# Optimization experiments

Measured on AMD Instinct MI355X. Metric: run time of the kernel, lower is better.

Reference implementation:

```python
import jax, jax.numpy as jnp
import numpy as np

EPS = 1e-5
N_HEAD = 16

def _ln(x, g, b):
    m = jnp.mean(x, -1, keepdims=True)
    v = jnp.mean((x - m) ** 2, -1, keepdims=True)
    return (x - m) * jax.lax.rsqrt(v + EPS) * g + b

def _mlp(x, fc_w, fc_b, proj_w, proj_b):
    h = x @ fc_w.T + fc_b
    h = h * jax.nn.sigmoid(1.702 * h)  # QuickGELU
    return h @ proj_w.T + proj_b

def setup_inputs() -> dict:
    key = jax.random.key(0)
    ks = jax.random.split(key, 16)
    S, B, D, BOX = 577, 8, 1024, 16
    sc = 0.02
    return {
        'x': jax.random.normal(ks[0], (S, B, D), jnp.float32),
        'detection_attn_mask': jax.random.normal(ks[1], (B * BOX * N_HEAD, 1, S), jnp.float32),
        'box_coords': jax.random.uniform(ks[2], (B, BOX, 4), jnp.float32),
        'layers': 24,
        'need_patch': 0,
        'in_proj_w': sc * jax.random.normal(ks[3], (3 * D, D), jnp.float32),
        'in_proj_b': jnp.zeros((3 * D,), jnp.float32),
        'out_w': sc * jax.random.normal(ks[4], (D, D), jnp.float32),
        'out_b': jnp.zeros((D,), jnp.float32),
        'ln1_g': jnp.ones((D,), jnp.float32),
        'ln1_b': jnp.zeros((D,), jnp.float32),
        'ln2_g': jnp.ones((D,), jnp.float32),
        'ln2_b': jnp.zeros((D,), jnp.float32),
        'fc_w': sc * jax.random.normal(ks[5], (4 * D, D), jnp.float32),
        'fc_b': jnp.zeros((4 * D,), jnp.float32),
        'proj_w': sc * jax.random.normal(ks[6], (D, 4 * D), jnp.float32),
        'proj_b': jnp.zeros((D,), jnp.float32),
    }

def reference(x, detection_attn_mask, box_coords, layers, need_patch,
              in_proj_w, in_proj_b, out_w, out_b,
              ln1_g, ln1_b, ln2_g, ln2_b, fc_w, fc_b, proj_w, proj_b):
    # step == layers-1, detection_attn_mask is not None, need_patch is False.
    S, B, D = x.shape
    H = N_HEAD
    hd = D // H
    BOX = box_coords.shape[1]  # uniform boxes per image

    h = _ln(x, ln1_g, ln1_b)                       # [S,B,D]
    qkv = h @ in_proj_w.T + in_proj_b              # [S,B,3D]
    q, k, v = jnp.split(qkv, 3, axis=-1)

    # query is sliced to the CLS token only (q[:, :1, :] after head split)
    q0 = q[0].reshape(B, H, hd) / jnp.sqrt(jnp.asarray(hd, x.dtype))  # [B,H,hd]
    kh = k.reshape(S, B, H, hd).transpose(1, 2, 0, 3)                 # [B,H,S,hd]
    vh = v.reshape(S, B, H, hd).transpose(1, 2, 0, 3)                 # [B,H,S,hd]

    attn = jnp.einsum('bhe,bhse->bhs', q0, kh)     # [B,H,S]

    # mask rows are ordered (batch, box, head); Nt == 1 is squeezed
    mask = detection_attn_mask.reshape(B, BOX, H, S)
    p_exp = jax.nn.softmax(attn[:, None] + mask, axis=-1)             # [B,BOX,H,S]
    out_exp = jnp.einsum('bxhs,bhse->bxhe', p_exp, vh).reshape(B * BOX, D)
    out_exp = out_exp @ out_w.T + out_b            # [B*BOX, D]

    p = jax.nn.softmax(attn, axis=-1)
    out = jnp.einsum('bhs,bhse->bhe', p, vh).reshape(B, D) @ out_w.T + out_b

    cls = x[0] + out                               # residual with CLS token
    cls = cls + _mlp(_ln(cls, ln2_g, ln2_b), fc_w, fc_b, proj_w, proj_b)

    x0_exp = jnp.repeat(x[0], BOX, axis=0)         # [B*BOX, D], batch-major
    mask_cls = x0_exp + out_exp
    mask_cls = mask_cls + _mlp(_ln(mask_cls, ln2_g, ln2_b), fc_w, fc_b, proj_w, proj_b)

    return mask_cls[None], cls[None]               # [1,B*BOX,D], [1,B,D]
```

## Files before the change

kernel.cpp:

```cpp
#include <hip/hip_runtime.h>
#include <stdint.h>

typedef unsigned short u16;
typedef unsigned int u32;
typedef __bf16 bf16x8 __attribute__((ext_vector_type(8)));
typedef float f32x4 __attribute__((ext_vector_type(4)));

#define LDT 72
#define HLD 516

__device__ __forceinline__ float bf2f(u16 u) {
  u32 v = ((u32)u) << 16;
  return __builtin_bit_cast(float, v);
}
__device__ __forceinline__ u16 f2bf(float f) {
  u32 u = __builtin_bit_cast(u32, f);
  u32 r = u + 0x7fffu + ((u >> 16) & 1u);
  return (u16)(r >> 16);
}

__device__ __forceinline__ float block_sum4(float v, float* red, int t) {
#pragma unroll
  for (int o = 32; o; o >>= 1) v += __shfl_xor(v, o, 64);
  if ((t & 63) == 0) red[t >> 6] = v;
  __syncthreads();
  float r = red[0] + red[1] + red[2] + red[3];
  __syncthreads();
  return r;
}

#define GLD16(gp, lp)                                                   \
  __builtin_amdgcn_global_load_lds(                                     \
      (const __attribute__((address_space(1))) void*)(gp),              \
      (__attribute__((address_space(3))) void*)(lp), 16, 0, 0)

__global__ __launch_bounds__(256) void cvt_ln(
    const float* __restrict__ WV, u16* __restrict__ WVD,
    const float* __restrict__ X, const float* __restrict__ G,
    const float* __restrict__ Bt, u16* __restrict__ O) {
  int t = threadIdx.x;
  if (blockIdx.x < 1024) {
    int i = blockIdx.x * 1024 + t * 4;
    float4 f = *(const float4*)(WV + i);
    u32 lo = (u32)f2bf(f.x) | ((u32)f2bf(f.y) << 16);
    u32 hi = (u32)f2bf(f.z) | ((u32)f2bf(f.w) << 16);
    uint2 val = {lo, hi};
    *(uint2*)(WVD + i) = val;
    return;
  }
  __shared__ float red[4];
  int row = blockIdx.x - 1024;
  float4 xv = *(const float4*)(X + (size_t)row * 1024 + t * 4);
  float v[4] = {xv.x, xv.y, xv.z, xv.w};
  float s = v[0] + v[1] + v[2] + v[3];
  s = block_sum4(s, red, t);
  float mean = s * (1.f / 1024.f);
  float q = 0.f;
#pragma unroll
  for (int i = 0; i < 4; ++i) { float d = v[i] - mean; q += d * d; }
  q = block_sum4(q, red, t);
  float rstd = rsqrtf(q * (1.f / 1024.f) + 1e-5f);
  float4 g = *(const float4*)(G + t * 4);
  float4 b = *(const float4*)(Bt + t * 4);
  float gg[4] = {g.x, g.y, g.z, g.w}, bb[4] = {b.x, b.y, b.z, b.w};
  u16 o[4];
#pragma unroll
  for (int i = 0; i < 4; ++i) o[i] = f2bf((v[i] - mean) * rstd * gg[i] + bb[i]);
  u32* op = (u32*)(O + (size_t)row * 1024 + t * 4);
  op[0] = (u32)o[0] | ((u32)o[1] << 16);
  op[1] = (u32)o[2] | ((u32)o[3] << 16);
}

__global__ __launch_bounds__(256) void vgemm_q(
    const u16* __restrict__ A, const u16* __restrict__ W,
    const float* __restrict__ bias, u16* __restrict__ C, int M,
    const float* __restrict__ WQ, const float* __restrict__ QB,
    const float* __restrict__ WK, const float* __restrict__ BK,
    u16* __restrict__ QW, float* __restrict__ C0) {
  int t = threadIdx.x;
  if (blockIdx.x < 296) {
    __shared__ u16 As[128 * 64];
    __shared__ u16 Bs[128 * 64];
    int lane = t & 63, wv = t >> 6;
    int bm = (blockIdx.x % 37) * 128, bn = (blockIdx.x / 37) * 128;
    int quad = lane >> 4, rlow = lane & 15;
    int lrow = lane >> 3, lcol = (lane & 7) * 8;
    int wrow = (wv & 1) * 64, wcol = (wv >> 1) * 64;
    f32x4 acc[4][4] = {};
    for (int k0 = 0; k0 < 1024; k0 += 64) {
      __syncthreads();
#pragma unroll
      for (int j = 0; j < 4; ++j) {
        int rb = j * 4 + wv;
        int row = rb * 8 + lrow;
        int gm = bm + row; if (gm >= M) gm = M - 1;
        GLD16(A + (size_t)gm * 1024 + k0 + lcol, &As[rb * 8 * 64]);
        int gn = bn + row;
        GLD16(W + (size_t)gn * 1024 + k0 + lcol, &Bs[rb * 8 * 64]);
      }
      __syncthreads();
#pragma unroll
      for (int kk = 0; kk < 64; kk += 32) {
        bf16x8 a[4], b[4];
#pragma unroll
        for (int i = 0; i < 4; ++i)
          a[i] = *(const bf16x8*)(&As[(wrow + i * 16 + rlow) * 64 + kk + quad * 8]);
#pragma unroll
        for (int j = 0; j < 4; ++j)
          b[j] = *(const bf16x8*)(&Bs[(wcol + j * 16 + rlow) * 64 + kk + quad * 8]);
#pragma unroll
        for (int i = 0; i < 4; ++i)
#pragma unroll
          for (int j = 0; j < 4; ++j)
            acc[i][j] = __builtin_amdgcn_mfma_f32_16x16x32_bf16(a[i], b[j], acc[i][j], 0, 0, 0);
      }
    }
#pragma unroll
    for (int j = 0; j < 4; ++j) {
      int gn = bn + wcol + j * 16 + rlow;
      float bv = bias[gn];
#pragma unroll
      for (int i = 0; i < 4; ++i)
#pragma unroll
        for (int r = 0; r < 4; ++r) {
          int gm = bm + wrow + i * 16 + quad * 4 + r;
          if (gm < M) C[(size_t)gm * 1024 + gn] = f2bf(acc[i][j][r] + bv);
        }
    }
    return;
  }
  __shared__ float hsf[1024];
  __shared__ float ps[256];
  __shared__ float qs[64];
  int bh = blockIdx.x - 296, b = bh >> 4, h = bh & 15;
  {
    uint2 two = *(const uint2*)(A + (size_t)b * 1024 + t * 4);
    hsf[t * 4 + 0] = bf2f(two.x & 0xffff);
    hsf[t * 4 + 1] = bf2f(two.x >> 16);
    hsf[t * 4 + 2] = bf2f(two.y & 0xffff);
    hsf[t * 4 + 3] = bf2f(two.y >> 16);
  }
  __syncthreads();
  {
    int n = t >> 2, part = t & 3;
    const float* wr = WQ + (size_t)(h * 64 + n) * 1024 + part * 256;
    const float* hp = hsf + part * 256;
    float acc = 0.f;
#pragma unroll 4
    for (int d = 0; d < 256; d += 4) {
      float4 w = *(const float4*)(wr + d);
      acc += w.x * hp[d] + w.y * hp[d + 1] + w.z * hp[d + 2] + w.w * hp[d + 3];
    }
    ps[t] = acc;
  }
  __syncthreads();
  if (t < 64) {
    float q = ps[t * 4] + ps[t * 4 + 1] + ps[t * 4 + 2] + ps[t * 4 + 3] + QB[h * 64 + t];
    qs[t] = q * 0.125f;
  }
  __syncthreads();
  float a4[4] = {0.f, 0.f, 0.f, 0.f};
  int d0 = t * 4;
#pragma unroll 4
  for (int n2 = 0; n2 < 64; ++n2) {
    float4 w = *(const float4*)(WK + (size_t)(h * 64 + n2) * 1024 + d0);
    float q = qs[n2];
    a4[0] += q * w.x; a4[1] += q * w.y; a4[2] += q * w.z; a4[3] += q * w.w;
  }
  u16 o[4];
#pragma unroll
  for (int i = 0; i < 4; ++i) o[i] = f2bf(a4[i]);
  u32* op = (u32*)(QW + (size_t)bh * 1024 + d0);
  op[0] = (u32)o[0] | ((u32)o[1] << 16);
  op[1] = (u32)o[2] | ((u32)o[3] << 16);
  if (t == 0) {
    float c = 0.f;
    for (int n2 = 0; n2 < 64; ++n2) c += qs[n2] * BK[h * 64 + n2];
    C0[bh] = c;
  }
}

__global__ __launch_bounds__(256) void gemm_bt_splitk_p(
    const u16* __restrict__ A, int lda, const float* __restrict__ Wf, int ldw,
    float* __restrict__ P, int pstride, int ldc, int M, int N, int KC) {
  __shared__ u16 As[64 * LDT];
  __shared__ u16 Bs[64 * LDT];
  int t = threadIdx.x;
  int bm = blockIdx.x * 64, bn = blockIdx.y * 64;
  int kbase = blockIdx.z * KC;
  float* PZ = P + (size_t)blockIdx.z * pstride;
  int lane = t & 63, wv = t >> 6;
  f32x4 acc[4] = {};
  int srow = t >> 3, scol = (t & 7) * 8;

  for (int k0 = kbase; k0 < kbase + KC; k0 += 64) {
    __syncthreads();
#pragma unroll
    for (int rr = 0; rr < 2; ++rr) {
      int r = srow + rr * 32;
      int gm = bm + r;
      uint4 da = {0, 0, 0, 0};
      if (gm < M) da = *(const uint4*)(A + (size_t)gm * lda + k0 + scol);
      *(uint4*)(&As[r * LDT + scol]) = da;
      int gn = bn + r;
      uint4 dw = {0, 0, 0, 0};
      if (gn < N) {
        const float* wr = Wf + (size_t)gn * ldw + k0 + scol;
        float4 w0 = *(const float4*)(wr);
        float4 w1 = *(const float4*)(wr + 4);
        dw.x = (u32)f2bf(w0.x) | ((u32)f2bf(w0.y) << 16);
        dw.y = (u32)f2bf(w0.z) | ((u32)f2bf(w0.w) << 16);
        dw.z = (u32)f2bf(w1.x) | ((u32)f2bf(w1.y) << 16);
        dw.w = (u32)f2bf(w1.z) | ((u32)f2bf(w1.w) << 16);
      }
      *(uint4*)(&Bs[r * LDT + scol]) = dw;
    }
    __syncthreads();
    int quad = lane >> 4, rlow = lane & 15;
#pragma unroll
    for (int kk = 0; kk < 64; kk += 32) {
      bf16x8 a = *(const bf16x8*)(&As[(wv * 16 + rlow) * LDT + kk + quad * 8]);
#pragma unroll
      for (int j = 0; j < 4; ++j) {
        bf16x8 b = *(const bf16x8*)(&Bs[(j * 16 + rlow) * LDT + kk + quad * 8]);
        acc[j] = __builtin_amdgcn_mfma_f32_16x16x32_bf16(a, b, acc[j], 0, 0, 0);
      }
    }
  }
  int quad = lane >> 4, cidx = lane & 15;
#pragma unroll
  for (int j = 0; j < 4; ++j) {
    int gn = bn + j * 16 + cidx;
#pragma unroll
    for (int r = 0; r < 4; ++r) {
      int gm = bm + wv * 16 + quad * 4 + r;
      if (gm < M && gn < N) PZ[(size_t)gm * ldc + gn] = acc[j][r];
    }
  }
}

__global__ __launch_bounds__(256) void resid_ln_red(
    const float* __restrict__ X, const float* __restrict__ OP,
    const float* __restrict__ OB, const float* __restrict__ G,
    const float* __restrict__ Bt, float* __restrict__ CLS, u16* __restrict__ H2) {
  __shared__ float red[4];
  const int PS = 136 * 1024;
  int row = blockIdx.x, t = threadIdx.x;
  int bi = (row < 128) ? (row >> 4) : (row - 128);
  float4 xv = *(const float4*)(X + (size_t)bi * 1024 + t * 4);
  float4 ob = *(const float4*)(OB + t * 4);
  float v[4] = {xv.x + ob.x, xv.y + ob.y, xv.z + ob.z, xv.w + ob.w};
#pragma unroll
  for (int z = 0; z < 8; ++z) {
    float4 pv = *(const float4*)(OP + (size_t)z * PS + (size_t)row * 1024 + t * 4);
    v[0] += pv.x; v[1] += pv.y; v[2] += pv.z; v[3] += pv.w;
  }
  float* cp = CLS + (size_t)row * 1024 + t * 4;
#pragma unroll
  for (int i = 0; i < 4; ++i) cp[i] = v[i];
  float s = v[0] + v[1] + v[2] + v[3];
  s = block_sum4(s, red, t);
  float mean = s * (1.f / 1024.f);
  float q = 0.f;
#pragma unroll
  for (int i = 0; i < 4; ++i) { float d = v[i] - mean; q += d * d; }
  q = block_sum4(q, red, t);
  float rstd = rsqrtf(q * (1.f / 1024.f) + 1e-5f);
  float4 g = *(const float4*)(G + t * 4);
  float4 b = *(const float4*)(Bt + t * 4);
  float gg[4] = {g.x, g.y, g.z, g.w}, bb[4] = {b.x, b.y, b.z, b.w};
  u16 o[4];
#pragma unroll
  for (int i = 0; i < 4; ++i) o[i] = f2bf((v[i] - mean) * rstd * gg[i] + bb[i]);
  u32* op = (u32*)(H2 + (size_t)row * 1024 + t * 4);
  op[0] = (u32)o[0] | ((u32)o[1] << 16);
  op[1] = (u32)o[2] | ((u32)o[3] << 16);
}

__global__ __launch_bounds__(256) void gelu_red(
    const float* __restrict__ FP, const float* __restrict__ FB,
    u16* __restrict__ O, int total) {
  const int PS = 136 * 4096;
  int i = (blockIdx.x * 256 + threadIdx.x) * 4;
  if (i < total) {
#pragma unroll
    for (int k = 0; k < 4; ++k) {
      int idx = i + k;
      float v = FB[idx & 4095];
#pragma unroll
      for (int z = 0; z < 4; ++z) v += FP[(size_t)z * PS + idx];
      O[idx] = f2bf(v / (1.f + __expf(-1.702f * v)));
    }
  }
}

__global__ __launch_bounds__(256) void final_red(
    const float* __restrict__ PP, const float* __restrict__ PB,
    const float* __restrict__ CLS, float* __restrict__ O, int total) {
  const int PS = 136 * 1024;
  int i = (blockIdx.x * 256 + threadIdx.x) * 4;
  if (i < total) {
#pragma unroll
    for (int k = 0; k < 4; ++k) {
      int idx = i + k;
      float v = PB[idx & 1023] + CLS[idx];
#pragma unroll
      for (int z = 0; z < 16; ++z) v += PP[(size_t)z * PS + idx];
      O[idx] = v;
    }
  }
}

__global__ __launch_bounds__(256) void attn_dot(
    const u16* __restrict__ H, const u16* __restrict__ QW,
    const float* __restrict__ C0, float* __restrict__ ATT) {
  __shared__ __align__(16) u32 Hs[16 * HLD];
  __shared__ __align__(16) u32 Qs[16 * HLD];
  int b = blockIdx.y, s0 = blockIdx.x * 16, t = threadIdx.x;
  for (int idx = t; idx < 16 * 512; idx += 256) {
    int row = idx >> 9, col = idx & 511;
    int s = s0 + row;
    u32 v = 0;
    if (s < 577) v = *(const u32*)(H + ((size_t)(s * 8 + b) << 10) + col * 2);
    Hs[row * HLD + col] = v;
    Qs[row * HLD + col] = *(const u32*)(QW + (size_t)(b * 16 + row) * 1024 + col * 2);
  }
  __syncthreads();
  int si = t & 15, hh = t >> 4;
  int s = s0 + si;
  if (s < 577) {
    const u32* hr = &Hs[si * HLD];
    const u32* qr = &Qs[hh * HLD];
    float a0 = 0.f, a1 = 0.f, a2 = 0.f, a3 = 0.f;
    for (int d = 0; d < 512; d += 8) {
      uint4 hv = *(const uint4*)(&hr[d]);
      uint4 qv = *(const uint4*)(&qr[d]);
      uint4 hw = *(const uint4*)(&hr[d + 4]);
      uint4 qw2 = *(const uint4*)(&qr[d + 4]);
      a0 += bf2f(hv.x & 0xffff) * bf2f(qv.x & 0xffff) + bf2f(hv.x >> 16) * bf2f(qv.x >> 16);
      a1 += bf2f(hv.y & 0xffff) * bf2f(qv.y & 0xffff) + bf2f(hv.y >> 16) * bf2f(qv.y >> 16);
      a2 += bf2f(hv.z & 0xffff) * bf2f(qv.z & 0xffff) + bf2f(hv.z >> 16) * bf2f(qv.z >> 16);
      a3 += bf2f(hv.w & 0xffff) * bf2f(qv.w & 0xffff) + bf2f(hv.w >> 16) * bf2f(qv.w >> 16);
      a0 += bf2f(hw.x & 0xffff) * bf2f(qw2.x & 0xffff) + bf2f(hw.x >> 16) * bf2f(qw2.x >> 16);
      a1 += bf2f(hw.y & 0xffff) * bf2f(qw2.y & 0xffff) + bf2f(hw.y >> 16) * bf2f(qw2.y >> 16);
      a2 += bf2f(hw.z & 0xffff) * bf2f(qw2.z & 0xffff) + bf2f(hw.z >> 16) * bf2f(qw2.z >> 16);
      a3 += bf2f(hw.w & 0xffff) * bf2f(qw2.w & 0xffff) + bf2f(hw.w >> 16) * bf2f(qw2.w >> 16);
    }
    ATT[(size_t)(b * 16 + hh) * 577 + s] = (a0 + a1) + (a2 + a3) + C0[b * 16 + hh];
  }
}

__global__ __launch_bounds__(256) void softmax_pv(
    const float* __restrict__ ATT, const float* __restrict__ MASK,
    const u16* __restrict__ V, u16* __restrict__ AO) {
  const int S = 577;
  int blk = blockIdx.x;
  int b = blk / 272, rem = blk % 272;
  int x = rem >> 4, h = rem & 15;
  __shared__ float p[S];
  __shared__ float redm[4];
  __shared__ float reds[4];
  __shared__ float partial[256];
  int t = threadIdx.x, lane = t & 63, wv = t >> 6;
  const float* arow = ATT + (size_t)(b * 16 + h) * S;
  float lmax = -3e38f;
  for (int s = t; s < S; s += 256) {
    float v = arow[s];
    if (x < 16) v += MASK[(size_t)((b * 16 + x) * 16 + h) * S + s];
    p[s] = v;
    lmax = fmaxf(lmax, v);
  }
#pragma unroll
  for (int o = 32; o; o >>= 1) lmax = fmaxf(lmax, __shfl_xor(lmax, o, 64));
  if (lane == 0) redm[wv] = lmax;
  __syncthreads();
  float m = fmaxf(fmaxf(redm[0], redm[1]), fmaxf(redm[2], redm[3]));
  float lsum = 0.f;
  for (int s = t; s < S; s += 256) {
    float e = __expf(p[s] - m);
    p[s] = e;
    lsum += e;
  }
#pragma unroll
  for (int o = 32; o; o >>= 1) lsum += __shfl_xor(lsum, o, 64);
  if (lane == 0) reds[wv] = lsum;
  __syncthreads();
  float inv = 1.f / (reds[0] + reds[1] + reds[2] + reds[3]);
  float acc = 0.f;
  const u16* vb = V + h * 64 + lane;
  int s = wv;
  for (; s + 28 < S; s += 32) {
    float w0 = p[s], w1 = p[s + 4], w2 = p[s + 8], w3 = p[s + 12];
    float w4 = p[s + 16], w5 = p[s + 20], w6 = p[s + 24], w7 = p[s + 28];
    float v0 = bf2f(vb[(size_t)((s)*8 + b) << 10]);
    float v1 = bf2f(vb[(size_t)((s + 4) * 8 + b) << 10]);
    float v2 = bf2f(vb[(size_t)((s + 8) * 8 + b) << 10]);
    float v3 = bf2f(vb[(size_t)((s + 12) * 8 + b) << 10]);
    float v4 = bf2f(vb[(size_t)((s + 16) * 8 + b) << 10]);
    float v5 = bf2f(vb[(size_t)((s + 20) * 8 + b) << 10]);
    float v6 = bf2f(vb[(size_t)((s + 24) * 8 + b) << 10]);
    float v7 = bf2f(vb[(size_t)((s + 28) * 8 + b) << 10]);
    acc += w0 * v0 + w1 * v1 + w2 * v2 + w3 * v3;
    acc += w4 * v4 + w5 * v5 + w6 * v6 + w7 * v7;
  }
  for (; s < S; s += 4) acc += p[s] * bf2f(vb[(size_t)(s * 8 + b) << 10]);
  partial[t] = acc;
  __syncthreads();
  if (t < 64) {
    float r = (partial[t] + partial[t + 64] + partial[t + 128] + partial[t + 192]) * inv;
    int row = (x < 16) ? (b * 16 + x) : (128 + b);
    AO[(size_t)row * 1024 + h * 64 + t] = f2bf(r);
  }
}

extern "C" void kernel_launch(void* const* d_in, const int* in_sizes, int n_in,
                              void* d_out, int out_size, void* d_ws, size_t ws_size,
                              hipStream_t stream) {
  const float* x      = (const float*)d_in[0];
  const float* mask   = (const float*)d_in[1];
  const float* in_w   = (const float*)d_in[5];
  const float* in_b   = (const float*)d_in[6];
  const float* out_w  = (const float*)d_in[7];
  const float* out_b  = (const float*)d_in[8];
  const float* ln1_g  = (const float*)d_in[9];
  const float* ln1_b  = (const float*)d_in[10];
  const float* ln2_g  = (const float*)d_in[11];
  const float* ln2_b  = (const float*)d_in[12];
  const float* fc_w   = (const float*)d_in[13];
  const float* fc_b   = (const float*)d_in[14];
  const float* proj_w = (const float*)d_in[15];
  const float* proj_b = (const float*)d_in[16];
  float* out = (float*)d_out;

  const int SB = 577 * 8;
  char* base = (char*)d_ws;
  size_t off = 0;
  auto alloc = [&](size_t bytes) {
    char* p = base + off;
    off += (bytes + 255) & ~(size_t)255;
    return p;
  };
  u16* wv_b     = (u16*)alloc((size_t)1024 * 1024 * 2);
  u16* h        = (u16*)alloc((size_t)SB * 1024 * 2);
  u16* v        = (u16*)alloc((size_t)SB * 1024 * 2);
  u16* qw       = (u16*)alloc(128 * 1024 * 2);
  float* c0     = (float*)alloc(128 * 4);
  float* attn   = (float*)alloc(128 * 577 * 4);
  u16* attn_out = (u16*)alloc(136 * 1024 * 2);
  float* Op     = (float*)alloc((size_t)8 * 136 * 1024 * 4);
  float* clspre = (float*)alloc(136 * 1024 * 4);
  u16* h2       = (u16*)alloc(136 * 1024 * 2);
  float* Fp     = (float*)alloc((size_t)4 * 136 * 4096 * 4);
  u16* hg       = (u16*)alloc((size_t)136 * 4096 * 2);
  float* Pp     = (float*)alloc((size_t)16 * 136 * 1024 * 4);

  cvt_ln<<<1024 + SB, 256, 0, stream>>>(in_w + (size_t)2048 * 1024, wv_b,
                                        x, ln1_g, ln1_b, h);
  vgemm_q<<<296 + 128, 256, 0, stream>>>(
      h, wv_b, in_b + 2048, v, SB,
      in_w, in_b, in_w + (size_t)1024 * 1024, in_b + 1024, qw, c0);
  attn_dot<<<dim3(37, 8), 256, 0, stream>>>(h, qw, c0, attn);
  softmax_pv<<<8 * 17 * 16, 256, 0, stream>>>(attn, mask, v, attn_out);
  gemm_bt_splitk_p<<<dim3(3, 16, 8), 256, 0, stream>>>(
      attn_out, 1024, out_w, 1024, Op, 136 * 1024, 1024, 136, 1024, 128);
  resid_ln_red<<<136, 256, 0, stream>>>(x, Op, out_b, ln2_g, ln2_b, clspre, h2);
  gemm_bt_splitk_p<<<dim3(3, 64, 4), 256, 0, stream>>>(
      h2, 1024, fc_w, 1024, Fp, 136 * 4096, 4096, 136, 4096, 256);
  gelu_red<<<544, 256, 0, stream>>>(Fp, fc_b, hg, 136 * 4096);
  gemm_bt_splitk_p<<<dim3(3, 16, 16), 256, 0, stream>>>(
      hg, 4096, proj_w, 4096, Pp, 136 * 1024, 1024, 136, 1024, 256);
  final_red<<<136, 256, 0, stream>>>(Pp, proj_b, clspre, out, 136 * 1024);

  (void)in_sizes; (void)n_in; (void)out_size; (void)ws_size;
}
```

Before: 244.2 us.

## Fuse split-K reduction and QuickGELU into proj GEMM A-tile load; halve split-K

Removes the separate gelu_red kernel. The proj GEMM now sums the four fc split-K partials, adds the bias, applies QuickGELU and converts to bf16 while staging its A tile, so the intermediate bf16 activation buffer is never written or read back. Split-K counts are halved for the out-proj GEMM (8 to 4) and the proj GEMM (16 to 8), which shrinks the partial buffers and the work in the downstream reductions. In exchange each proj block recomputes GELU for its A tile across the three... actually across all 16 N-blocks, and with fewer split-K slices each block does a longer K loop, so there is less parallelism.

New measurement: 255.9 us. +4.8%, slower.

```diff
diff --git a/kernel.cpp b/kernel.cpp
--- a/kernel.cpp
+++ b/kernel.cpp
@@ -239,6 +239,88 @@
   }
 }
 
+__global__ __launch_bounds__(256) void gemm_proj_fused(
+    const float* __restrict__ FP, const float* __restrict__ FB,
+    const float* __restrict__ Wf,
+    float* __restrict__ P, int pstride, int M, int KC) {
+  const int FPS = 136 * 4096;
+  __shared__ u16 As[64 * LDT];
+  __shared__ u16 Bs[64 * LDT];
+  int t = threadIdx.x;
+  int bm = blockIdx.x * 64, bn = blockIdx.y * 64;
+  int kbase = blockIdx.z * KC;
+  float* PZ = P + (size_t)blockIdx.z * pstride;
+  int lane = t & 63, wv = t >> 6;
+  f32x4 acc[4] = {};
+  int srow = t >> 3, scol = (t & 7) * 8;
+
+  for (int k0 = kbase; k0 < kbase + KC; k0 += 64) {
+    __syncthreads();
+#pragma unroll
+    for (int rr = 0; rr < 2; ++rr) {
+      int r = srow + rr * 32;
+      int gm = bm + r;
+      uint4 da = {0, 0, 0, 0};
+      if (gm < M) {
+        int col = k0 + scol;
+        float vv[8];
+        float4 b0 = *(const float4*)(FB + col);
+        float4 b1 = *(const float4*)(FB + col + 4);
+        vv[0] = b0.x; vv[1] = b0.y; vv[2] = b0.z; vv[3] = b0.w;
+        vv[4] = b1.x; vv[5] = b1.y; vv[6] = b1.z; vv[7] = b1.w;
+#pragma unroll
+        for (int z = 0; z < 4; ++z) {
+          const float* fp = FP + (size_t)z * FPS + (size_t)gm * 4096 + col;
+          float4 p0 = *(const float4*)(fp);
+          float4 p1 = *(const float4*)(fp + 4);
+          vv[0] += p0.x; vv[1] += p0.y; vv[2] += p0.z; vv[3] += p0.w;
+          vv[4] += p1.x; vv[5] += p1.y; vv[6] += p1.z; vv[7] += p1.w;
+        }
+        u16 g[8];
+#pragma unroll
+        for (int e = 0; e < 8; ++e)
+          g[e] = f2bf(vv[e] / (1.f + __expf(-1.702f * vv[e])));
+        da.x = (u32)g[0] | ((u32)g[1] << 16);
+        da.y = (u32)g[2] | ((u32)g[3] << 16);
+        da.z = (u32)g[4] | ((u32)g[5] << 16);
+        da.w = (u32)g[6] | ((u32)g[7] << 16);
+      }
+      *(uint4*)(&As[r * LDT + scol]) = da;
+      int gn = bn + r;
+      const float* wr = Wf + (size_t)gn * 4096 + k0 + scol;
+      float4 w0 = *(const float4*)(wr);
+      float4 w1 = *(const float4*)(wr + 4);
+      uint4 dw;
+      dw.x = (u32)f2bf(w0.x) | ((u32)f2bf(w0.y) << 16);
+      dw.y = (u32)f2bf(w0.z) | ((u32)f2bf(w0.w) << 16);
+      dw.z = (u32)f2bf(w1.x) | ((u32)f2bf(w1.y) << 16);
+      dw.w = (u32)f2bf(w1.z) | ((u32)f2bf(w1.w) << 16);
+      *(uint4*)(&Bs[r * LDT + scol]) = dw;
+    }
+    __syncthreads();
+    int quad = lane >> 4, rlow = lane & 15;
+#pragma unroll
+    for (int kk = 0; kk < 64; kk += 32) {
+      bf16x8 a = *(const bf16x8*)(&As[(wv * 16 + rlow) * LDT + kk + quad * 8]);
+#pragma unroll
+      for (int j = 0; j < 4; ++j) {
+        bf16x8 b = *(const bf16x8*)(&Bs[(j * 16 + rlow) * LDT + kk + quad * 8]);
+        acc[j] = __builtin_amdgcn_mfma_f32_16x16x32_bf16(a, b, acc[j], 0, 0, 0);
+      }
+    }
+  }
+  int quad = lane >> 4, cidx = lane & 15;
+#pragma unroll
+  for (int j = 0; j < 4; ++j) {
+    int gn = bn + j * 16 + cidx;
+#pragma unroll
+    for (int r = 0; r < 4; ++r) {
+      int gm = bm + wv * 16 + quad * 4 + r;
+      if (gm < M) PZ[(size_t)gm * 1024 + gn] = acc[j][r];
+    }
+  }
+}
+
 __global__ __launch_bounds__(256) void resid_ln_red(
     const float* __restrict__ X, const float* __restrict__ OP,
     const float* __restrict__ OB, const float* __restrict__ G,
@@ -251,7 +333,7 @@
   float4 ob = *(const float4*)(OB + t * 4);
   float v[4] = {xv.x + ob.x, xv.y + ob.y, xv.z + ob.z, xv.w + ob.w};
 #pragma unroll
-  for (int z = 0; z < 8; ++z) {
+  for (int z = 0; z < 4; ++z) {
     float4 pv = *(const float4*)(OP + (size_t)z * PS + (size_t)row * 1024 + t * 4);
     v[0] += pv.x; v[1] += pv.y; v[2] += pv.z; v[3] += pv.w;
   }
@@ -277,23 +359,6 @@
   op[1] = (u32)o[2] | ((u32)o[3] << 16);
 }
 
-__global__ __launch_bounds__(256) void gelu_red(
-    const float* __restrict__ FP, const float* __restrict__ FB,
-    u16* __restrict__ O, int total) {
-  const int PS = 136 * 4096;
-  int i = (blockIdx.x * 256 + threadIdx.x) * 4;
-  if (i < total) {
-#pragma unroll
-    for (int k = 0; k < 4; ++k) {
-      int idx = i + k;
-      float v = FB[idx & 4095];
-#pragma unroll
-      for (int z = 0; z < 4; ++z) v += FP[(size_t)z * PS + idx];
-      O[idx] = f2bf(v / (1.f + __expf(-1.702f * v)));
-    }
-  }
-}
-
 __global__ __launch_bounds__(256) void final_red(
     const float* __restrict__ PP, const float* __restrict__ PB,
     const float* __restrict__ CLS, float* __restrict__ O, int total) {
@@ -305,7 +370,7 @@
       int idx = i + k;
       float v = PB[idx & 1023] + CLS[idx];
 #pragma unroll
-      for (int z = 0; z < 16; ++z) v += PP[(size_t)z * PS + idx];
+      for (int z = 0; z < 8; ++z) v += PP[(size_t)z * PS + idx];
       O[idx] = v;
     }
   }
@@ -447,12 +512,11 @@
   float* c0     = (float*)alloc(128 * 4);
   float* attn   = (float*)alloc(128 * 577 * 4);
   u16* attn_out = (u16*)alloc(136 * 1024 * 2);
-  float* Op     = (float*)alloc((size_t)8 * 136 * 1024 * 4);
+  float* Op     = (float*)alloc((size_t)4 * 136 * 1024 * 4);
   float* clspre = (float*)alloc(136 * 1024 * 4);
   u16* h2       = (u16*)alloc(136 * 1024 * 2);
   float* Fp     = (float*)alloc((size_t)4 * 136 * 4096 * 4);
-  u16* hg       = (u16*)alloc((size_t)136 * 4096 * 2);
-  float* Pp     = (float*)alloc((size_t)16 * 136 * 1024 * 4);
+  float* Pp     = (float*)alloc((size_t)8 * 136 * 1024 * 4);
 
   cvt_ln<<<1024 + SB, 256, 0, stream>>>(in_w + (size_t)2048 * 1024, wv_b,
                                         x, ln1_g, ln1_b, h);
@@ -461,14 +525,13 @@
       in_w, in_b, in_w + (size_t)1024 * 1024, in_b + 1024, qw, c0);
   attn_dot<<<dim3(37, 8), 256, 0, stream>>>(h, qw, c0, attn);
   softmax_pv<<<8 * 17 * 16, 256, 0, stream>>>(attn, mask, v, attn_out);
-  gemm_bt_splitk_p<<<dim3(3, 16, 8), 256, 0, stream>>>(
-      attn_out, 1024, out_w, 1024, Op, 136 * 1024, 1024, 136, 1024, 128);
+  gemm_bt_splitk_p<<<dim3(3, 16, 4), 256, 0, stream>>>(
+      attn_out, 1024, out_w, 1024, Op, 136 * 1024, 1024, 136, 1024, 256);
   resid_ln_red<<<136, 256, 0, stream>>>(x, Op, out_b, ln2_g, ln2_b, clspre, h2);
   gemm_bt_splitk_p<<<dim3(3, 64, 4), 256, 0, stream>>>(
       h2, 1024, fc_w, 1024, Fp, 136 * 4096, 4096, 136, 4096, 256);
-  gelu_red<<<544, 256, 0, stream>>>(Fp, fc_b, hg, 136 * 4096);
-  gemm_bt_splitk_p<<<dim3(3, 16, 16), 256, 0, stream>>>(
-      hg, 4096, proj_w, 4096, Pp, 136 * 1024, 1024, 136, 1024, 256);
+  gemm_proj_fused<<<dim3(3, 16, 8), 256, 0, stream>>>(
+      Fp, fc_b, proj_w, Pp, 136 * 1024, 136, 512);
   final_red<<<136, 256, 0, stream>>>(Pp, proj_b, clspre, out, 136 * 1024);
 
   (void)in_sizes; (void)n_in; (void)out_size; (void)ws_size;
```
